# Optimization experiments

Measured on AMD Instinct MI355X. Metric: run time of the kernel, lower is better.

Reference implementation:

```python
import jax, jax.numpy as jnp
import numpy as np

B, S, D = 128, 256, 128
VOCAB, NH, K = 21, 4, 4
DI = 2 * D            # mLSTM inner dim (proj_factor=2)
QKB = 8               # qkv_proj_blocksize
NB = DI // QKB        # 32 block-diagonal qkv blocks
DHM = DI // NH        # 64 = mLSTM head dim
DHS = D // NH         # 32 = sLSTM head dim
FFU = 2 * D           # gated FFN up dim (proj_factor=2.0)


def _ln(x, w, eps=1e-5):
    mu = x.mean(-1, keepdims=True)
    var = x.var(-1, keepdims=True)
    return (x - mu) / jnp.sqrt(var + eps) * w


def _mh_ln(x, w, nh, eps=1e-5):
    # multi-head (group) layernorm: normalize each head's channels, scale by per-channel w
    b, s, d = x.shape
    xh = x.reshape(b, s, nh, d // nh)
    mu = xh.mean(-1, keepdims=True)
    var = xh.var(-1, keepdims=True)
    xn = (xh - mu) / jnp.sqrt(var + eps)
    return xn.reshape(b, s, d) * w


def _causal_conv(x, w, bias):
    # depthwise causal conv1d: x (B,S,C), w (C,K), left-pad K-1
    s = x.shape[1]
    k = w.shape[1]
    xp = jnp.pad(x, ((0, 0), (k - 1, 0), (0, 0)))
    return sum(xp[:, j:j + s, :] * w[:, j] for j in range(k)) + bias


def _blockdiag(x, w):
    # block-diagonal (headwise) linear: x (B,S,D), w (nb, out_per_block, in_per_block)
    b, s, d = x.shape
    nb = w.shape[0]
    xh = x.reshape(b, s, nb, d // nb)
    return jnp.einsum('bshd,hed->bshe', xh, w).reshape(b, s, -1)


def _mlstm_parallel(q, k, v, ip, fp, eps=1e-6):
    # parallel stabilized mLSTM; q,k,v (B,NH,S,DH); ip,fp (B,NH,S,1)
    b, nh, s, dh = q.shape
    log_f = jax.nn.log_sigmoid(fp)
    lf_cum = jnp.concatenate([jnp.zeros((b, nh, 1, 1), q.dtype),
                              jnp.cumsum(log_f, axis=2)], axis=2)      # (B,NH,S+1,1)
    m = lf_cum - jnp.swapaxes(lf_cum, -2, -1)                          # (B,NH,S+1,S+1)
    ltr = jnp.tril(jnp.ones((s, s), bool))
    log_fg = jnp.where(ltr, m[:, :, 1:, 1:], -jnp.inf)
    log_d = log_fg + jnp.swapaxes(ip, -2, -1)                          # (B,NH,S,S)
    max_d = jnp.max(log_d, axis=-1, keepdims=True)
    dmat = jnp.exp(log_d - max_d)
    qk = jnp.einsum('bhqd,bhkd->bhqk', q, k) / (dh ** 0.5)
    c = qk * dmat
    norm = jnp.maximum(jnp.abs(c.sum(-1, keepdims=True)), jnp.exp(-max_d))
    return jnp.einsum('bhqk,bhkd->bhqd', c / (norm + eps), v)


def _slstm_scan(gi, gf, gz, go, rec_w, bias):
    # sLSTM recurrence; g* (B,S,NH,DH); rec_w (NH,DH,4*DH); bias (NH,4*DH)
    b, s, nh, dh = gi.shape
    bi, bf, bz, bo = jnp.split(bias, 4, axis=-1)

    def step(carry, inp):
        h, c, n, m = carry
        ixt, fxt, zxt, oxt = inp
        rec = jnp.einsum('bhd,hde->bhe', h, rec_w)
        ri, rf, rz, ro = jnp.split(rec, 4, axis=-1)
        iraw = ixt + ri + bi
        fraw = fxt + rf + bf
        zraw = zxt + rz + bz
        oraw = oxt + ro + bo
        logfplusm = m + jax.nn.log_sigmoid(fraw)
        mnew = jnp.maximum(iraw, logfplusm)
        ig = jnp.exp(iraw - mnew)
        fg = jnp.exp(logfplusm - mnew)
        cnew = fg * c + ig * jnp.tanh(zraw)
        nnew = fg * n + ig
        hnew = jax.nn.sigmoid(oraw) * cnew / nnew
        return (hnew, cnew, nnew, mnew), hnew

    init = tuple(jnp.zeros((b, nh, dh), gi.dtype) for _ in range(4))
    xs = tuple(jnp.moveaxis(t, 1, 0) for t in (gi, gf, gz, go))
    _, ys = jax.lax.scan(step, init, xs)
    return jnp.moveaxis(ys, 0, 1)  # (B,S,NH,DH)


def _forward(x, emb, m_ln_w, m_up_w, m_conv_w, m_conv_b, m_q_w, m_k_w, m_v_w,
             m_ig_w, m_ig_b, m_fg_w, m_fg_b, m_on_w, m_skip, m_down_w,
             s_ln1_w, s_conv_w, s_conv_b, s_ig_w, s_fg_w, s_zg_w, s_og_w,
             s_rec_w, s_bias, s_gn_w, s_ln2_w, s_ff_up_w, s_ff_down_w,
             post_norm_w):
    h = emb[x]  # (B,S,D)
    # ---- block 0: mLSTM block (pre-LN residual) ----
    xn = _ln(h, m_ln_w)
    x_in, z = jnp.split(xn @ m_up_w.T, 2, axis=-1)          # each (B,S,DI)
    xca = jax.nn.silu(_causal_conv(x_in, m_conv_w, m_conv_b))
    q = _blockdiag(xca, m_q_w)
    kk = _blockdiag(xca, m_k_w)
    v = _blockdiag(x_in, m_v_w)
    ifin = jnp.concatenate([q, kk, v], axis=-1)             # (B,S,3*DI)
    ip = jnp.swapaxes(ifin @ m_ig_w.T + m_ig_b, 1, 2)[..., None]  # (B,NH,S,1)
    fp = jnp.swapaxes(ifin @ m_fg_w.T + m_fg_b, 1, 2)[..., None]
    to_heads = lambda t: jnp.swapaxes(t.reshape(B, S, NH, DHM), 1, 2)
    ht = _mlstm_parallel(to_heads(q), to_heads(kk), to_heads(v), ip, fp)
    hm = jnp.swapaxes(ht, 1, 2).reshape(B, S, DI)
    hm = _mh_ln(hm, m_on_w, NH)
    hm = (hm + m_skip * xca) * jax.nn.silu(z)
    h = h + hm @ m_down_w.T
    # ---- blocks 1,2: sLSTM blocks (pre-LN residual + gated gelu FFN) ----
    for i in range(2):
        xn = _ln(h, s_ln1_w[i])
        xc = jax.nn.silu(_causal_conv(xn, s_conv_w[i], s_conv_b[i]))
        gi = _blockdiag(xc, s_ig_w[i]).reshape(B, S, NH, DHS)
        gf = _blockdiag(xc, s_fg_w[i]).reshape(B, S, NH, DHS)
        gz = _blockdiag(xn, s_zg_w[i]).reshape(B, S, NH, DHS)
        go = _blockdiag(xn, s_og_w[i]).reshape(B, S, NH, DHS)
        y = _slstm_scan(gi, gf, gz, go, s_rec_w[i], s_bias[i])
        h = h + _mh_ln(y.reshape(B, S, D), s_gn_w[i], NH)
        xn2 = _ln(h, s_ln2_w[i])
        gate, up = jnp.split(xn2 @ s_ff_up_w[i].T, 2, axis=-1)
        h = h + (jax.nn.gelu(gate, approximate=False) * up) @ s_ff_down_w[i].T
    return _ln(h, post_norm_w)


def setup_inputs():
    key = jax.random.key(0)
    ks = iter(jax.random.split(key, 64))
    r = lambda shape, s=0.02: jax.random.normal(next(ks), shape, jnp.float32) * s
    inp = {}
    inp['x'] = jax.random.randint(next(ks), (B, S), 0, VOCAB)
    inp['emb'] = r((VOCAB, D)).at[0].set(0.0)  # padding_idx=0
    inp['m_ln_w'] = jnp.ones((D,), jnp.float32)
    inp['m_up_w'] = r((2 * DI, D))
    inp['m_conv_w'] = r((DI, K), 0.1)
    inp['m_conv_b'] = jnp.zeros((DI,), jnp.float32)
    inp['m_q_w'] = r((NB, QKB, QKB), 0.1)
    inp['m_k_w'] = r((NB, QKB, QKB), 0.1)
    inp['m_v_w'] = r((NB, QKB, QKB), 0.1)
    inp['m_ig_w'] = r((NH, 3 * DI))
    inp['m_ig_b'] = r((NH,), 0.1)
    inp['m_fg_w'] = r((NH, 3 * DI))
    inp['m_fg_b'] = jnp.linspace(3.0, 6.0, NH)  # forget-gate bias init
    inp['m_on_w'] = jnp.ones((DI,), jnp.float32)
    inp['m_skip'] = jnp.ones((DI,), jnp.float32)
    inp['m_down_w'] = r((D, DI))
    inp['s_ln1_w'] = jnp.ones((2, D), jnp.float32)
    inp['s_conv_w'] = r((2, D, K), 0.1)
    inp['s_conv_b'] = jnp.zeros((2, D), jnp.float32)
    inp['s_ig_w'] = r((2, NH, DHS, DHS), 0.05)
    inp['s_fg_w'] = r((2, NH, DHS, DHS), 0.05)
    inp['s_zg_w'] = r((2, NH, DHS, DHS), 0.05)
    inp['s_og_w'] = r((2, NH, DHS, DHS), 0.05)
    inp['s_rec_w'] = r((2, NH, DHS, 4 * DHS), 0.05)
    inp['s_bias'] = jnp.zeros((2, NH, 4 * DHS), jnp.float32).at[:, :, DHS:2 * DHS].set(jnp.linspace(3.0, 6.0, DHS))
    inp['s_gn_w'] = jnp.ones((2, D), jnp.float32)
    inp['s_ln2_w'] = jnp.ones((2, D), jnp.float32)
    inp['s_ff_up_w'] = r((2, 2 * FFU, D))
    inp['s_ff_down_w'] = r((2, D, FFU))
    inp['post_norm_w'] = jnp.ones((D,), jnp.float32)
    return inp


def reference(x, emb, m_ln_w, m_up_w, m_conv_w, m_conv_b, m_q_w, m_k_w, m_v_w,
              m_ig_w, m_ig_b, m_fg_w, m_fg_b, m_on_w, m_skip, m_down_w,
              s_ln1_w, s_conv_w, s_conv_b, s_ig_w, s_fg_w, s_zg_w, s_og_w,
              s_rec_w, s_bias, s_gn_w, s_ln2_w, s_ff_up_w, s_ff_down_w,
              post_norm_w):
    return _forward(x, emb, m_ln_w, m_up_w, m_conv_w, m_conv_b, m_q_w, m_k_w, m_v_w,
                    m_ig_w, m_ig_b, m_fg_w, m_fg_b, m_on_w, m_skip, m_down_w,
                    s_ln1_w, s_conv_w, s_conv_b, s_ig_w, s_fg_w, s_zg_w, s_og_w,
                    s_rec_w, s_bias, s_gn_w, s_ln2_w, s_ff_up_w, s_ff_down_w,
                    post_norm_w)
```

## Files before the change

### kernel.cpp

```cpp
#include <hip/hip_runtime.h>
#include <hip/hip_bf16.h>

#define BB 128
#define SS 256
#define DD 128
#define DI 256
#define NH 4
#define DHM 64
#define DHS 32
#define NROWS (BB*SS)

#define WAVE_SYNC() do { asm volatile("s_waitcnt lgkmcnt(0)" ::: "memory"); __builtin_amdgcn_wave_barrier(); } while (0)

typedef __attribute__((ext_vector_type(8))) short short8;
typedef __attribute__((ext_vector_type(4))) float f32x4;
typedef __attribute__((ext_vector_type(2))) int i32x2;

__device__ __forceinline__ float sigmoidf_(float x) { return 1.f / (1.f + __expf(-x)); }
__device__ __forceinline__ float siluf_(float x) { return x / (1.f + __expf(-x)); }
__device__ __forceinline__ float logsigf_(float x) {
    return (x >= 0.f) ? -log1pf(__expf(-x)) : x - log1pf(__expf(x));
}
__device__ __forceinline__ float geluf_(float g) {
    return 0.5f * g * (1.f + erff(g * 0.70710678118654752f));
}
__device__ __forceinline__ ushort bf16u(float x) {
    unsigned u = __float_as_uint(x);
    u += 0x7fffu + ((u >> 16) & 1u);
    return (ushort)(u >> 16);
}
__device__ __forceinline__ float ubf(ushort v) {
    return __uint_as_float((unsigned)v << 16);
}
__device__ __forceinline__ float rdlane(float v, int lane) {
    return __int_as_float(__builtin_amdgcn_readlane(__float_as_int(v), lane));
}
#define DPPADD(x, ctrl) ((x) + __int_as_float(__builtin_amdgcn_update_dpp(0, __float_as_int(x), (ctrl), 0xf, 0xf, true)))

__global__ __launch_bounds__(256) void wprep_kernel(const float* __restrict__ m_up_w,
        const float* __restrict__ m_down_w, const float* __restrict__ s_ff_up_w,
        const float* __restrict__ s_ff_down_w, const float* __restrict__ wi,
        const float* __restrict__ wf, const float* __restrict__ wz,
        const float* __restrict__ wo, const float* __restrict__ igw,
        const float* __restrict__ fgw,
        ushort* __restrict__ upb, ushort* __restrict__ downb,
        ushort* __restrict__ ffupb, ushort* __restrict__ ffdownb,
        ushort* __restrict__ sgwb, ushort* __restrict__ w16b) {
    int gid = blockIdx.x * 256 + threadIdx.x;
    if (gid < 65536) {
        upb[gid] = bf16u(m_up_w[gid]);
    } else if (gid < 98304) {
        int i = gid - 65536;
        downb[i] = bf16u(m_down_w[i]);
    } else if (gid < 229376) {
        int i = gid - 98304;
        ffupb[i] = bf16u(s_ff_up_w[i]);
    } else if (gid < 294912) {
        int i = gid - 229376;
        ffdownb[i] = bf16u(s_ff_down_w[i]);
    } else if (gid < 557056) {
        int idx = gid - 294912;
        int t = idx & 127;
        int oc = (idx >> 7) & 255;
        int pair = (idx >> 15) & 1;
        int i2 = idx >> 16;
        int h = oc >> 6, l = oc & 63, gate = (l >> 5) & 1, e = l & 31;
        const float* w = pair == 0 ? (gate == 0 ? wi : wf) : (gate == 0 ? wz : wo);
        float val = ((t >> 5) == h) ? w[i2 * 4096 + h * 1024 + e * 32 + (t & 31)] : 0.f;
        sgwb[idx] = bf16u(val);
    } else if (gid < 569344) {
        int idx = gid - 557056;
        int t = idx % 768, j = idx / 768;
        float v = 0.f;
        if (j < 4) v = igw[j * 768 + t];
        else if (j < 8) v = fgw[(j - 4) * 768 + t];
        w16b[idx] = bf16u(v);
    }
}

__global__ __launch_bounds__(256) void embed_ln_kernel(const int* __restrict__ x,
        const float* __restrict__ emb, const float* __restrict__ w,
        float* __restrict__ h, ushort* __restrict__ outb) {
    int row = blockIdx.x * 4 + (threadIdx.x >> 6);
    int lane = threadIdx.x & 63;
    int tok = x[row];
    float a = emb[tok * DD + lane], b = emb[tok * DD + 64 + lane];
    h[(size_t)row * DD + lane] = a;
    h[(size_t)row * DD + 64 + lane] = b;
    float s1 = a + b, s2 = a * a + b * b;
    #pragma unroll
    for (int o = 32; o; o >>= 1) { s1 += __shfl_xor(s1, o); s2 += __shfl_xor(s2, o); }
    float mu = s1 * (1.f / 128.f);
    float var = s2 * (1.f / 128.f) - mu * mu;
    float inv = rsqrtf(var + 1e-5f);
    ushort* brow = outb + (size_t)row * DD;
    brow[lane] = bf16u((a - mu) * inv * w[lane]);
    brow[lane + 64] = bf16u((b - mu) * inv * w[lane + 64]);
}

__global__ __launch_bounds__(256) void ln128_kernel(const float* __restrict__ x,
        const float* __restrict__ w, float* __restrict__ out, ushort* __restrict__ outb) {
    int row = blockIdx.x * 4 + (threadIdx.x >> 6);
    int lane = threadIdx.x & 63;
    const float* xr = x + (size_t)row * DD;
    float a = xr[lane], b = xr[lane + 64];
    float s1 = a + b, s2 = a * a + b * b;
    #pragma unroll
    for (int o = 32; o; o >>= 1) { s1 += __shfl_xor(s1, o); s2 += __shfl_xor(s2, o); }
    float mu = s1 * (1.f / 128.f);
    float var = s2 * (1.f / 128.f) - mu * mu;
    float inv = rsqrtf(var + 1e-5f);
    float va = (a - mu) * inv * w[lane];
    float vb = (b - mu) * inv * w[lane + 64];
    if (out) {
        float* orow = out + (size_t)row * DD;
        orow[lane] = va; orow[lane + 64] = vb;
    }
    if (outb) {
        ushort* brow = outb + (size_t)row * DD;
        brow[lane] = bf16u(va); brow[lane + 64] = bf16u(vb);
    }
}

__global__ __launch_bounds__(256) void ln_conv_s_kernel(const float* __restrict__ hsrc,
        const float* __restrict__ lnw, const float* __restrict__ cw,
        const float* __restrict__ cb, ushort* __restrict__ xnb, ushort* __restrict__ xcb) {
    __shared__ ushort lnbuf[67][128];
    int blk = blockIdx.x;
    int st = blk & 3, b = blk >> 2;
    int r0 = st * 64;
    int tid = threadIdx.x;
    int wv = tid >> 6, lane = tid & 63;
    #pragma unroll
    for (int p = 0; p < 17; ++p) {
        int rl = p * 4 + wv;
        if (rl < 67) {
            int s = r0 - 3 + rl;
            if (s >= 0) {
                const float* xr = hsrc + ((size_t)(b * 256 + s)) * 128;
                float a = xr[lane], c2 = xr[lane + 64];
                float s1 = a + c2, s2 = a * a + c2 * c2;
                #pragma unroll
                for (int o = 32; o; o >>= 1) { s1 += __shfl_xor(s1, o); s2 += __shfl_xor(s2, o); }
                float mu = s1 * (1.f / 128.f);
                float var = s2 * (1.f / 128.f) - mu * mu;
                float inv = rsqrtf(var + 1e-5f);
                lnbuf[rl][lane] = bf16u((a - mu) * inv * lnw[lane]);
                lnbuf[rl][lane + 64] = bf16u((c2 - mu) * inv * lnw[lane + 64]);
            } else {
                lnbuf[rl][lane] = 0;
                lnbuf[rl][lane + 64] = 0;
            }
        }
    }
    __syncthreads();
    int ch = tid & 127;
    int half = tid >> 7;
    float w0 = cw[ch * 4 + 0], w1 = cw[ch * 4 + 1], w2 = cw[ch * 4 + 2], w3 = cw[ch * 4 + 3];
    float bias = cb[ch];
    #pragma unroll 4
    for (int i = 0; i < 32; ++i) {
        int rr = half * 32 + i;
        int rl = 3 + rr;
        float acc = bias
            + ubf(lnbuf[rl - 3][ch]) * w0
            + ubf(lnbuf[rl - 2][ch]) * w1
            + ubf(lnbuf[rl - 1][ch]) * w2
            + ubf(lnbuf[rl][ch]) * w3;
        size_t gr = (size_t)(b * 256 + r0 + rr);
        xcb[gr * 128 + ch] = bf16u(siluf_(acc));
        xnb[gr * 128 + ch] = lnbuf[rl][ch];
    }
}

__global__ __launch_bounds__(256, 2) void gemm_bf16_kernel(const ushort* __restrict__ A, int lda,
        const ushort* __restrict__ W, float* __restrict__ C, ushort* __restrict__ Cb,
        int ldc, int K, int addC) {
    __shared__ ushort As[128 * 32];
    __shared__ ushort Bs[128 * 32];
    int m0 = blockIdx.x * 128;
    int n0 = blockIdx.y * 128;
    int tid = threadIdx.x;
    int wv = tid >> 6, l = tid & 63;
    int lr = l & 15, lg = l >> 4, g4 = lg * 4;
    int wr = wv >> 1, wc = wv & 1;
    int sr = tid >> 1;
    int sc = (tid & 1) * 2;

    f32x4 acc[4][4] = {};
    for (int k0 = 0; k0 < K; k0 += 32) {
        __syncthreads();
        #pragma unroll
        for (int u = 0; u < 2; ++u) {
            int c = sc + u;
            uint4 av = *(const uint4*)(A + (size_t)(m0 + sr) * lda + k0 + c * 8);
            *(uint4*)(As + sr * 32 + ((c ^ (sr & 3)) * 8)) = av;
            uint4 wv4 = *(const uint4*)(W + (size_t)(n0 + sr) * K + k0 + c * 8);
            *(uint4*)(Bs + sr * 32 + ((c ^ (sr & 3)) * 8)) = wv4;
        }
        __syncthreads();
        short8 af[4], bf[4];
        #pragma unroll
        for (int fm = 0; fm < 4; ++fm) {
            int row = wr * 64 + fm * 16 + lr;
            af[fm] = *(const short8*)(As + row * 32 + ((lg ^ (row & 3)) * 8));
        }
        #pragma unroll
        for (int fn = 0; fn < 4; ++fn) {
            int row = wc * 64 + fn * 16 + lr;
            bf[fn] = *(const short8*)(Bs + row * 32 + ((lg ^ (row & 3)) * 8));
        }
        #pragma unroll
        for (int fm = 0; fm < 4; ++fm)
            #pragma unroll
            for (int fn = 0; fn < 4; ++fn)
                acc[fm][fn] = __builtin_amdgcn_mfma_f32_16x16x32_bf16(af[fm], bf[fn], acc[fm][fn], 0, 0, 0);
    }
    #pragma unroll
    for (int fm = 0; fm < 4; ++fm) {
        #pragma unroll
        for (int fn = 0; fn < 4; ++fn) {
            #pragma unroll
            for (int r = 0; r < 4; ++r) {
                size_t idx = (size_t)(m0 + wr * 64 + fm * 16 + g4 + r) * ldc + n0 + wc * 64 + fn * 16 + lr;
                if (Cb) Cb[idx] = bf16u(acc[fm][fn][r]);
                else if (addC) C[idx] += acc[fm][fn][r];
                else C[idx] = acc[fm][fn][r];
            }
        }
    }
}

__global__ __launch_bounds__(256, 2) void sgate_gemm_kernel(const ushort* __restrict__ xcb,
        const ushort* __restrict__ xnb, const ushort* __restrict__ Wif,
        const ushort* __restrict__ Wzo, ushort* __restrict__ gifb, ushort* __restrict__ gzob) {
    __shared__ ushort As[128 * 32];
    __shared__ ushort Bs[128 * 32];
    int y = blockIdx.y;
    const ushort* A = (y < 2) ? xcb : xnb;
    const ushort* W = (y < 2) ? Wif : Wzo;
    ushort* Cb = (y < 2) ? gifb : gzob;
    int m0 = blockIdx.x * 128;
    int n0 = (y & 1) * 128;
    int tid = threadIdx.x;
    int wv = tid >> 6, l = tid & 63;
    int lr = l & 15, lg = l >> 4, g4 = lg * 4;
    int wr = wv >> 1, wc = wv & 1;
    int sr = tid >> 1;
    int sc = (tid & 1) * 2;

    f32x4 acc[4][4] = {};
    for (int k0 = 0; k0 < 128; k0 += 32) {
        __syncthreads();
        #pragma unroll
        for (int u = 0; u < 2; ++u) {
            int c = sc + u;
            uint4 av = *(const uint4*)(A + (size_t)(m0 + sr) * 128 + k0 + c * 8);
            *(uint4*)(As + sr * 32 + ((c ^ (sr & 3)) * 8)) = av;
            uint4 wv4 = *(const uint4*)(W + (size_t)(n0 + sr) * 128 + k0 + c * 8);
            *(uint4*)(Bs + sr * 32 + ((c ^ (sr & 3)) * 8)) = wv4;
        }
        __syncthreads();
        short8 af[4], bf[4];
        #pragma unroll
        for (int fm = 0; fm < 4; ++fm) {
            int row = wr * 64 + fm * 16 + lr;
            af[fm] = *(const short8*)(As + row * 32 + ((lg ^ (row & 3)) * 8));
        }
        #pragma unroll
        for (int fn = 0; fn < 4; ++fn) {
            int row = wc * 64 + fn * 16 + lr;
            bf[fn] = *(const short8*)(Bs + row * 32 + ((lg ^ (row & 3)) * 8));
        }
        #pragma unroll
        for (int fm = 0; fm < 4; ++fm)
            #pragma unroll
            for (int fn = 0; fn < 4; ++fn)
                acc[fm][fn] = __builtin_amdgcn_mfma_f32_16x16x32_bf16(af[fm], bf[fn], acc[fm][fn], 0, 0, 0);
    }
    #pragma unroll
    for (int fm = 0; fm < 4; ++fm)
        #pragma unroll
        for (int fn = 0; fn < 4; ++fn)
            #pragma unroll
            for (int r = 0; r < 4; ++r) {
                size_t idx = (size_t)(m0 + wr * 64 + fm * 16 + g4 + r) * 256 + n0 + wc * 64 + fn * 16 + lr;
                Cb[idx] = bf16u(acc[fm][fn][r]);
            }
}

__global__ __launch_bounds__(256, 2) void gemm_glu_kernel(const ushort* __restrict__ xzb,
        const ushort* __restrict__ W, float* __restrict__ C) {
    __shared__ ushort As[128 * 32];
    __shared__ ushort Bs[128 * 32];
    int m0 = blockIdx.x * 128;
    int tid = threadIdx.x;
    int wv = tid >> 6, l = tid & 63;
    int lr = l & 15, lg = l >> 4, g4 = lg * 4;
    int wr = wv >> 1, wc = wv & 1;
    int sr = tid >> 1;
    int sc = (tid & 1) * 2;

    f32x4 acc[4][4] = {};
    for (int k0 = 0; k0 < 256; k0 += 32) {
        __syncthreads();
        #pragma unroll
        for (int u = 0; u < 2; ++u) {
            int c = sc + u;
            short8 g8 = *(const short8*)(xzb + (size_t)(m0 + sr) * 512 + k0 + c * 8);
            short8 u8 = *(const short8*)(xzb + (size_t)(m0 + sr) * 512 + 256 + k0 + c * 8);
            short8 o8;
            #pragma unroll
            for (int t = 0; t < 8; ++t)
                o8[t] = (short)bf16u(geluf_(ubf((ushort)g8[t])) * ubf((ushort)u8[t]));
            *(short8*)(As + sr * 32 + ((c ^ (sr & 3)) * 8)) = o8;
            uint4 wv4 = *(const uint4*)(W + (size_t)sr * 256 + k0 + c * 8);
            *(uint4*)(Bs + sr * 32 + ((c ^ (sr & 3)) * 8)) = wv4;
        }
        __syncthreads();
        short8 af[4], bf[4];
        #pragma unroll
        for (int fm = 0; fm < 4; ++fm) {
            int row = wr * 64 + fm * 16 + lr;
            af[fm] = *(const short8*)(As + row * 32 + ((lg ^ (row & 3)) * 8));
        }
        #pragma unroll
        for (int fn = 0; fn < 4; ++fn) {
            int row = wc * 64 + fn * 16 + lr;
            bf[fn] = *(const short8*)(Bs + row * 32 + ((lg ^ (row & 3)) * 8));
        }
        #pragma unroll
        for (int fm = 0; fm < 4; ++fm)
            #pragma unroll
            for (int fn = 0; fn < 4; ++fn)
                acc[fm][fn] = __builtin_amdgcn_mfma_f32_16x16x32_bf16(af[fm], bf[fn], acc[fm][fn], 0, 0, 0);
    }
    #pragma unroll
    for (int fm = 0; fm < 4; ++fm)
        #pragma unroll
        for (int fn = 0; fn < 4; ++fn)
            #pragma unroll
            for (int r = 0; r < 4; ++r) {
                size_t idx = (size_t)(m0 + wr * 64 + fm * 16 + g4 + r) * 128 + wc * 64 + fn * 16 + lr;
                C[idx] += acc[fm][fn][r];
            }
}

__global__ __launch_bounds__(256) void gategemm_kernel(const ushort* __restrict__ qb,
        const ushort* __restrict__ kb, const ushort* __restrict__ vb,
        const ushort* __restrict__ W16, const float* __restrict__ igb,
        const float* __restrict__ fgb, float* __restrict__ ip, float* __restrict__ fp) {
    int tid = threadIdx.x;
    int wv = tid >> 6, l = tid & 63;
    int lr = l & 15, lg = l >> 4, g4 = lg * 4;
    int row0 = blockIdx.x * 128 + wv * 32;
    f32x4 acc[2] = {};
    #pragma unroll
    for (int k0 = 0; k0 < 768; k0 += 32) {
        short8 bfr = *(const short8*)(W16 + lr * 768 + k0 + lg * 8);
        #pragma unroll
        for (int mi = 0; mi < 2; ++mi) {
            int row = row0 + mi * 16 + lr;
            int b = row >> 8, s = row & 255;
            const ushort* src;
            size_t addr;
            if (k0 < 256) {
                src = qb;
                addr = ((size_t)(b * 4 + (k0 >> 6)) * 256 + s) * 64 + (k0 & 63) + lg * 8;
            } else if (k0 < 512) {
                int kq = k0 - 256;
                src = kb;
                addr = ((size_t)(b * 4 + (kq >> 6)) * 256 + s) * 64 + (kq & 63) + lg * 8;
            } else {
                src = vb;
                addr = (size_t)row * 256 + (k0 - 512) + lg * 8;
            }
            short8 afr = *(const short8*)(src + addr);
            acc[mi] = __builtin_amdgcn_mfma_f32_16x16x32_bf16(afr, bfr, acc[mi], 0, 0, 0);
        }
    }
    if (lr < 8) {
        float bias = (lr < 4) ? igb[lr] : fgb[lr - 4];
        float* dst = (lr < 4) ? ip : fp;
        int hh = lr & 3;
        #pragma unroll
        for (int mi = 0; mi < 2; ++mi) {
            #pragma unroll
            for (int r = 0; r < 4; ++r) {
                int row = row0 + mi * 16 + g4 + r;
                int b = row >> 8, s = row & 255;
                dst[(size_t)(b * 4 + hh) * 256 + s] = acc[mi][r] + bias;
            }
        }
    }
}

__global__ __launch_bounds__(256) void mqkv_kernel(const ushort* __restrict__ xzb,
        const float* __restrict__ cw, const float* __restrict__ cb,
        const float* __restrict__ qw, const float* __restrict__ kw,
        const float* __restrict__ vw, ushort* __restrict__ xcab,
        ushort* __restrict__ qb16, ushort* __restrict__ kb16,
        ushort* __restrict__ vb16) {
    int gid = blockIdx.x * 256 + threadIdx.x;
    int oct = gid & 31;
    int row = gid >> 5;
    int s = row & 255;
    int b = row >> 8;
    float xin[4][8];
    #pragma unroll
    for (int j = 0; j < 4; ++j) {
        int ss = s - 3 + j;
        if (ss >= 0) {
            short8 v8 = *(const short8*)(xzb + ((size_t)row + j - 3) * 512 + oct * 8);
            #pragma unroll
            for (int t = 0; t < 8; ++t) xin[j][t] = ubf((ushort)v8[t]);
        } else {
            #pragma unroll
            for (int t = 0; t < 8; ++t) xin[j][t] = 0.f;
        }
    }
    float xc8[8];
    #pragma unroll
    for (int t = 0; t < 8; ++t) {
        int ch = oct * 8 + t;
        float acc = cb[ch];
        #pragma unroll
        for (int j = 0; j < 4; ++j) acc += xin[j][t] * cw[ch * 4 + j];
        xc8[t] = siluf_(acc);
    }
    short8 qs, ks, vs, xs;
    #pragma unroll
    for (int e = 0; e < 8; ++e) {
        const float* qw8 = qw + (size_t)(oct * 8 + e) * 8;
        const float* kw8 = kw + (size_t)(oct * 8 + e) * 8;
        const float* vw8 = vw + (size_t)(oct * 8 + e) * 8;
        float aq = 0.f, ak = 0.f, av = 0.f;
        #pragma unroll
        for (int t = 0; t < 8; ++t) {
            aq += xc8[t] * qw8[t];
            ak += xc8[t] * kw8[t];
            av += xin[3][t] * vw8[t];
        }
        qs[e] = (short)bf16u(aq);
        ks[e] = (short)bf16u(ak);
        vs[e] = (short)bf16u(av);
        xs[e] = (short)bf16u(xc8[e]);
    }
    *(short8*)(xcab + (size_t)row * 256 + oct * 8) = xs;
    *(short8*)(vb16 + (size_t)row * 256 + oct * 8) = vs;
    int h2 = oct >> 3, dd = (oct & 7) * 8;
    size_t be = ((size_t)(b * 4 + h2) * 256 + s) * 64 + dd;
    *(short8*)(qb16 + be) = qs;
    *(short8*)(kb16 + be) = ks;
}

__global__ __launch_bounds__(64) void mprep_kernel(const float* __restrict__ ip,
        const float* __restrict__ fp, float* __restrict__ L,
        float* __restrict__ E, float* __restrict__ PM) {
    int bh = blockIdx.x;
    int lane = threadIdx.x;
    size_t base = (size_t)bh * SS + lane * 4;
    float lsv[4], ipv[4];
    #pragma unroll
    for (int u = 0; u < 4; ++u) {
        lsv[u] = logsigf_(fp[base + u]);
        ipv[u] = ip[base + u];
    }
    float p0 = lsv[0], p1 = p0 + lsv[1], p2 = p1 + lsv[2], p3 = p2 + lsv[3];
    float inc = p3;
    #pragma unroll
    for (int o = 1; o < 64; o <<= 1) {
        float wv = __shfl_up(inc, o);
        if (lane >= o) inc += wv;
    }
    float excl = inc - p3;
    float Lv[4] = {excl + p0, excl + p1, excl + p2, excl + p3};
    float Ev[4];
    #pragma unroll
    for (int u = 0; u < 4; ++u) Ev[u] = ipv[u] - Lv[u];
    float q0 = Ev[0], q1 = fmaxf(q0, Ev[1]), q2 = fmaxf(q1, Ev[2]), q3 = fmaxf(q2, Ev[3]);
    float incm = q3;
    #pragma unroll
    for (int o = 1; o < 64; o <<= 1) {
        float wv = __shfl_up(incm, o);
        if (lane >= o) incm = fmaxf(incm, wv);
    }
    float exm = __shfl_up(incm, 1);
    if (lane == 0) exm = -INFINITY;
    float qv[4] = {q0, q1, q2, q3};
    #pragma unroll
    for (int u = 0; u < 4; ++u) {
        L[base + u] = Lv[u];
        E[base + u] = Ev[u];
        PM[base + u] = fmaxf(exm, qv[u]);
    }
}

__global__ __launch_bounds__(256) void vtrans_kernel(const ushort* __restrict__ vb,
        ushort* __restrict__ vt) {
    int blk = blockIdx.x;
    int st = blk & 3, bh = blk >> 2;
    int b = bh >> 2, h = bh & 3;
    int tid = threadIdx.x;
    __shared__ ushort tile[64][68];
    int s0 = st * 64;
    #pragma unroll
    for (int u = 0; u < 16; ++u) {
        int idx = u * 256 + tid;
        int sl = idx >> 6, dl = idx & 63;
        tile[sl][dl] = vb[((size_t)(b * 256 + s0 + sl)) * 256 + h * 64 + dl];
    }
    __syncthreads();
    #pragma unroll
    for (int u = 0; u < 16; ++u) {
        int idx = u * 256 + tid;
        int dl = idx >> 6, sl = idx & 63;
        vt[((size_t)bh * 64 + dl) * 256 + s0 + sl] = tile[sl][dl];
    }
}

__global__ __launch_bounds__(256, 2) void mlstm_mfma_kernel(
        const ushort* __restrict__ qb, const ushort* __restrict__ kb,
        const ushort* __restrict__ vt, const float* __restrict__ Lg,
        const float* __restrict__ Eg, const float* __restrict__ PMg,
        const ushort* __restrict__ xzb, const ushort* __restrict__ xcab,
        const float* __restrict__ onw, const float* __restrict__ skip,
        ushort* __restrict__ outb) {
    int bh = blockIdx.x;
    int b = bh >> 2, h = bh & 3;
    int tid = threadIdx.x;
    int wv = tid >> 6, l = tid & 63;
    int lr = l & 15, lg = l >> 4, g4 = lg * 4;

    __shared__ ushort Kb[16384];
    __shared__ ushort Vt[16384];
    __shared__ ushort Pl[4 * 640];
    __shared__ float sE[SS], sPM[SS], sL[SS];

    const size_t gb16 = (size_t)bh * 16384;
    #pragma unroll
    for (int p2 = 0; p2 < 8; ++p2) {
        int id = p2 * 256 + tid;
        int r = id >> 3, c = id & 7;
        uint4 kval = *(const uint4*)(kb + gb16 + r * 64 + c * 8);
        *(uint4*)(Kb + r * 64 + ((c ^ (r & 7)) * 8)) = kval;
        int d = id >> 5, c2 = id & 31;
        uint4 vval = *(const uint4*)(vt + gb16 + d * 256 + c2 * 8);
        *(uint4*)(Vt + d * 256 + ((c2 ^ (d & 7)) * 8)) = vval;
    }
    sE[tid]  = Eg[(size_t)bh * SS + tid];
    sPM[tid] = PMg[(size_t)bh * SS + tid];
    sL[tid]  = Lg[(size_t)bh * SS + tid];
    __syncthreads();

    float onwv[4], skipv[4];
    #pragma unroll
    for (int dc = 0; dc < 4; ++dc) {
        int ch = h * 64 + dc * 16 + lr;
        onwv[dc] = onw[ch];
        skipv[dc] = skip[ch];
    }

    f32x4 O[4][4] = {};
    float csum[4][4] = {};
    const int pmap[4] = {wv, 7 - wv, 8 + wv, 15 - wv};
    ushort* Pw = Pl + wv * 640;

    #pragma unroll
    for (int rf = 0; rf < 4; ++rf) {
        int p = pmap[rf];
        int r0 = p * 16;
        short8 qf0 = *(const short8*)(qb + gb16 + (r0 + lr) * 64 + lg * 8);
        short8 qf1 = *(const short8*)(qb + gb16 + (r0 + lr) * 64 + 32 + lg * 8);
        float pmv[4], lv[4];
        #pragma unroll
        for (int r = 0; r < 4; ++r) { pmv[r] = sPM[r0 + g4 + r]; lv[r] = sL[r0 + g4 + r]; }
        int jtmax = r0 >> 5;
        #pragma unroll 1
        for (int jt = 0; jt <= jtmax; ++jt) {
            int jb = jt * 32;
            f32x4 s0 = {0.f, 0.f, 0.f, 0.f}, s1 = {0.f, 0.f, 0.f, 0.f};
            {
                int j = jb + lr;
                int sw = j & 7;
                short8 k00 = *(const short8*)(Kb + j * 64 + ((lg)     ^ sw) * 8);
                short8 k01 = *(const short8*)(Kb + j * 64 + ((4 + lg) ^ sw) * 8);
                int j2 = jb + 16 + lr;
                int sw2 = j2 & 7;
                short8 k10 = *(const short8*)(Kb + j2 * 64 + ((lg)     ^ sw2) * 8);
                short8 k11 = *(const short8*)(Kb + j2 * 64 + ((4 + lg) ^ sw2) * 8);
                s0 = __builtin_amdgcn_mfma_f32_16x16x32_bf16(qf0, k00, s0, 0, 0, 0);
                s0 = __builtin_amdgcn_mfma_f32_16x16x32_bf16(qf1, k01, s0, 0, 0, 0);
                s1 = __builtin_amdgcn_mfma_f32_16x16x32_bf16(qf0, k10, s1, 0, 0, 0);
                s1 = __builtin_amdgcn_mfma_f32_16x16x32_bf16(qf1, k11, s1, 0, 0, 0);
            }
            float e0 = sE[jb + lr], e1 = sE[jb + 16 + lr];
            int j0 = jb + lr, j1 = jb + 16 + lr;
            #pragma unroll
            for (int r = 0; r < 4; ++r) {
                int i = r0 + g4 + r;
                float sc0 = (j0 <= i) ? s0[r] * 0.125f * __expf(e0 - pmv[r]) : 0.f;
                float sc1 = (j1 <= i) ? s1[r] * 0.125f * __expf(e1 - pmv[r]) : 0.f;
                csum[rf][r] += sc0 + sc1;
                Pw[(g4 + r) * 40 + lr] = bf16u(sc0);
                Pw[(g4 + r) * 40 + 16 + lr] = bf16u(sc1);
            }
            WAVE_SYNC();
            short8 pf = *(const short8*)(Pw + lr * 40 + lg * 8);
            #pragma unroll
            for (int dc = 0; dc < 4; ++dc) {
                int d = dc * 16 + lr;
                int chunk = (jt * 4 + lg) ^ (d & 7);
                short8 vf = *(const short8*)(Vt + d * 256 + chunk * 8);
                O[rf][dc] = __builtin_amdgcn_mfma_f32_16x16x32_bf16(pf, vf, O[rf][dc], 0, 0, 0);
            }
        }
        #pragma unroll
        for (int r = 0; r < 4; ++r) {
            float cs = csum[rf][r];
            cs += __shfl_xor(cs, 1); cs += __shfl_xor(cs, 2);
            cs += __shfl_xor(cs, 4); cs += __shfl_xor(cs, 8);
            float nrm = fmaxf(fabsf(cs), __expf(-(lv[r] + pmv[r]))) + 1e-6f;
            float rinv = 1.f / nrm;
            float v0 = O[rf][0][r] * rinv, v1 = O[rf][1][r] * rinv;
            float v2 = O[rf][2][r] * rinv, v3 = O[rf][3][r] * rinv;
            float s1m = v0 + v1 + v2 + v3;
            float s2m = v0 * v0 + v1 * v1 + v2 * v2 + v3 * v3;
            s1m += __shfl_xor(s1m, 1); s2m += __shfl_xor(s2m, 1);
            s1m += __shfl_xor(s1m, 2); s2m += __shfl_xor(s2m, 2);
            s1m += __shfl_xor(s1m, 4); s2m += __shfl_xor(s2m, 4);
            s1m += __shfl_xor(s1m, 8); s2m += __shfl_xor(s2m, 8);
            float mu = s1m * (1.f / 64.f);
            float var = s2m * (1.f / 64.f) - mu * mu;
            float inv = rsqrtf(var + 1e-5f);
            int grow = b * 256 + r0 + g4 + r;
            float vv[4] = {v0, v1, v2, v3};
            #pragma unroll
            for (int dc = 0; dc < 4; ++dc) {
                int ch = h * 64 + dc * 16 + lr;
                float z = ubf(xzb[(size_t)grow * 512 + 256 + ch]);
                float xnv = (vv[dc] - mu) * inv * onwv[dc];
                float val = (xnv + skipv[dc] * ubf(xcab[(size_t)grow * 256 + ch])) * siluf_(z);
                outb[(size_t)grow * 256 + ch] = bf16u(val);
            }
        }
    }
}

__global__ __launch_bounds__(64, 1) void slstm_scan_kernel(const ushort* __restrict__ gifb,
        const ushort* __restrict__ gzob, const float* __restrict__ rec_w,
        const float* __restrict__ bias, const float* __restrict__ gnw,
        float* __restrict__ hbuf) {
    int bh = blockIdx.x;
    int b = bh >> 2, h = bh & 3;
    int l = threadIdx.x;
    int c = l & 31;
    bool lo = (l < 32);
    unsigned wpk[32];
    const float* wp = rec_w + (size_t)h * 4096 + l;
    #pragma unroll
    for (int d = 0; d < 32; ++d) {
        float w0v = wp[d * 128];
        float w1v = wp[d * 128 + 64];
        wpk[d] = ((unsigned)bf16u(w1v) << 16) | (unsigned)bf16u(w0v);
    }
    float b0 = bias[h * 128 + l];
    float b1 = bias[h * 128 + 64 + l];
    float gw = gnw[h * 32 + c];
    float cst = 0.f, nst = 0.f, hreg = 0.f;
    size_t gb = (size_t)b * SS * 256 + h * 64 + l;
    size_t hb = (size_t)b * SS * 128 + h * 32 + c;
    float pg0[4], pg1[4], ph[4];
    #pragma unroll
    for (int u = 0; u < 4; ++u) {
        pg0[u] = ubf(gifb[gb + (size_t)u * 256]);
        pg1[u] = ubf(gzob[gb + (size_t)u * 256]);
        ph[u]  = hbuf[hb + (size_t)u * 128];
    }
    float pend_hv = 0.f, pend_hcur = 0.f;
    int pend_off = 0;
    for (int s = 0; s < SS; s += 4) {
        #pragma unroll
        for (int u = 0; u < 4; ++u) {
            float a00 = 0.f, a01 = 0.f, a02 = 0.f, a03 = 0.f;
            float a10 = 0.f, a11 = 0.f, a12 = 0.f, a13 = 0.f;
            #pragma unroll
            for (int d = 0; d < 32; d += 4) {
                float h0 = rdlane(hreg, d);
                float h1 = rdlane(hreg, d + 1);
                float h2 = rdlane(hreg, d + 2);
                float h3 = rdlane(hreg, d + 3);
                unsigned p0 = wpk[d], p1 = wpk[d + 1], p2 = wpk[d + 2], p3 = wpk[d + 3];
                a00 += __uint_as_float(p0 << 16) * h0;
                a10 += __uint_as_float(p0) * h0;
                a01 += __uint_as_float(p1 << 16) * h1;
                a11 += __uint_as_float(p1) * h1;
                a02 += __uint_as_float(p2 << 16) * h2;
                a12 += __uint_as_float(p2) * h2;
                a03 += __uint_as_float(p3 << 16) * h3;
                a13 += __uint_as_float(p3) * h3;
            }
            float raw0 = pg0[u] + ((a00 + a01) + (a02 + a03)) + b0;
            float raw1 = pg1[u] + ((a10 + a11) + (a12 + a13)) + b1;
            float hcur = ph[u];
            {
                float s1 = pend_hv, s2 = pend_hv * pend_hv;
                s1 = DPPADD(s1, 0x111); s2 = DPPADD(s2, 0x111);
                s1 = DPPADD(s1, 0x112); s2 = DPPADD(s2, 0x112);
                s1 = DPPADD(s1, 0x114); s2 = DPPADD(s2, 0x114);
                s1 = DPPADD(s1, 0x118); s2 = DPPADD(s2, 0x118);
                s1 = DPPADD(s1, 0x142); s2 = DPPADD(s2, 0x142);
                s1 = DPPADD(s1, 0x143); s2 = DPPADD(s2, 0x143);
                float mu = rdlane(s1, 63) * (1.f / 64.f);
                float var = rdlane(s2, 63) * (1.f / 64.f) - mu * mu;
                float outv = (pend_hv - mu) * rsqrtf(var + 1e-5f) * gw;
                if (lo) hbuf[hb + (size_t)pend_off * 128] = pend_hcur + outv;
            }
            int s4 = s + 4 + u;
            if (s4 < SS) {
                pg0[u] = ubf(gifb[gb + (size_t)s4 * 256]);
                pg1[u] = ubf(gzob[gb + (size_t)s4 * 256]);
                ph[u]  = hbuf[hb + (size_t)s4 * 128];
            }
            i32x2 r0p = __builtin_amdgcn_permlane32_swap(__float_as_int(raw0), __float_as_int(raw0), false, false);
            i32x2 r1p = __builtin_amdgcn_permlane32_swap(__float_as_int(raw1), __float_as_int(raw1), false, false);
            float q0 = __int_as_float(lo ? r0p.y : r0p.x);
            float q1 = __int_as_float(lo ? r1p.y : r1p.x);
            float iraw = lo ? raw0 : q0;
            float zraw = lo ? raw1 : q1;
            float fraw = lo ? q0 : raw0;
            float oraw = lo ? q1 : raw1;
            float fg = __builtin_amdgcn_rcpf(1.f + __expf(-fraw));
            float ig = __expf(iraw);
            float e2z = __expf(2.f * zraw);
            float tz = 1.f - 2.f * __builtin_amdgcn_rcpf(e2z + 1.f);
            cst = fg * cst + ig * tz;
            nst = fg * nst + ig;
            float sg = __builtin_amdgcn_rcpf(1.f + __expf(-oraw));
            float hv = sg * cst * __builtin_amdgcn_rcpf(nst);
            hreg = hv;
            pend_hv = hv;
            pend_hcur = hcur;
            pend_off = s + u;
        }
    }
    {
        float s1 = pend_hv, s2 = pend_hv * pend_hv;
        s1 = DPPADD(s1, 0x111); s2 = DPPADD(s2, 0x111);
        s1 = DPPADD(s1, 0x112); s2 = DPPADD(s2, 0x112);
        s1 = DPPADD(s1, 0x114); s2 = DPPADD(s2, 0x114);
        s1 = DPPADD(s1, 0x118); s2 = DPPADD(s2, 0x118);
        s1 = DPPADD(s1, 0x142); s2 = DPPADD(s2, 0x142);
        s1 = DPPADD(s1, 0x143); s2 = DPPADD(s2, 0x143);
        float mu = rdlane(s1, 63) * (1.f / 64.f);
        float var = rdlane(s2, 63) * (1.f / 64.f) - mu * mu;
        float outv = (pend_hv - mu) * rsqrtf(var + 1e-5f) * gw;
        if (lo) hbuf[hb + (size_t)pend_off * 128] = pend_hcur + outv;
    }
}

extern "C" void kernel_launch(void* const* d_in, const int* in_sizes, int n_in,
                              void* d_out, int out_size, void* d_ws, size_t ws_size,
                              hipStream_t stream) {
    const int*   x        = (const int*)d_in[0];
    const float* emb      = (const float*)d_in[1];
    const float* m_ln_w   = (const float*)d_in[2];
    const float* m_up_w   = (const float*)d_in[3];
    const float* m_conv_w = (const float*)d_in[4];
    const float* m_conv_b = (const float*)d_in[5];
    const float* m_q_w    = (const float*)d_in[6];
    const float* m_k_w    = (const float*)d_in[7];
    const float* m_v_w    = (const float*)d_in[8];
    const float* m_ig_w   = (const float*)d_in[9];
    const float* m_ig_b   = (const float*)d_in[10];
    const float* m_fg_w   = (const float*)d_in[11];
    const float* m_fg_b   = (const float*)d_in[12];
    const float* m_on_w   = (const float*)d_in[13];
    const float* m_skip   = (const float*)d_in[14];
    const float* m_down_w = (const float*)d_in[15];
    const float* s_ln1_w  = (const float*)d_in[16];
    const float* s_conv_w = (const float*)d_in[17];
    const float* s_conv_b = (const float*)d_in[18];
    const float* s_ig_w   = (const float*)d_in[19];
    const float* s_fg_w   = (const float*)d_in[20];
    const float* s_zg_w   = (const float*)d_in[21];
    const float* s_og_w   = (const float*)d_in[22];
    const float* s_rec_w  = (const float*)d_in[23];
    const float* s_bias   = (const float*)d_in[24];
    const float* s_gn_w   = (const float*)d_in[25];
    const float* s_ln2_w  = (const float*)d_in[26];
    const float* s_ff_up_w   = (const float*)d_in[27];
    const float* s_ff_down_w = (const float*)d_in[28];
    const float* post_norm_w = (const float*)d_in[29];
    float* out = (float*)d_out;

    float* ws = (float*)d_ws;
    const size_t NR = NROWS;
    float* h   = ws;
    float* regA = h   + NR * 128;
    float* regB = regA + NR * 128;
    float* gip = regB + NR * 128;
    float* gfp = gip + 512 * 256;
    float* gL  = gfp + 512 * 256;
    float* gE  = gL  + 512 * 256;
    float* gPM = gE  + 512 * 256;
    float* extra = gPM + 512 * 256;
    ushort* xnb   = (ushort*)extra;
    ushort* xzb   = xnb + NR * 128;
    ushort* xcab  = xzb + NR * 512;
    ushort* qb16  = xcab + NR * 256;
    ushort* vb16  = qb16 + NR * 256;
    ushort* upb   = vb16 + NR * 256;
    ushort* downb = upb + 512 * 128;
    ushort* ffupb = downb + 128 * 256;
    ushort* ffdownb = ffupb + 2 * 512 * 128;
    ushort* sgwb  = ffdownb + 2 * 128 * 256;
    ushort* w16b  = sgwb + 2 * 2 * 256 * 128;
    ushort* kb16   = (ushort*)out;
    ushort* vtb    = (ushort*)regA;
    ushort* gifb   = (ushort*)regA;
    ushort* mpostb = (ushort*)regB;
    ushort* gzob   = (ushort*)regB;
    ushort* xcb    = qb16;

    wprep_kernel<<<(569344 + 255) / 256, 256, 0, stream>>>(m_up_w, m_down_w, s_ff_up_w,
            s_ff_down_w, s_ig_w, s_fg_w, s_zg_w, s_og_w, m_ig_w, m_fg_w,
            upb, downb, ffupb, ffdownb, sgwb, w16b);

    embed_ln_kernel<<<NR / 4, 256, 0, stream>>>(x, emb, m_ln_w, h, xnb);
    gemm_bf16_kernel<<<dim3(NR / 128, 4), 256, 0, stream>>>(xnb, 128, upb, nullptr, xzb, 512, 128, 0);
    mqkv_kernel<<<(NR * 32) / 256, 256, 0, stream>>>(xzb, m_conv_w, m_conv_b,
            m_q_w, m_k_w, m_v_w, xcab, qb16, kb16, vb16);
    gategemm_kernel<<<NR / 128, 256, 0, stream>>>(qb16, kb16, vb16, w16b, m_ig_b, m_fg_b, gip, gfp);
    mprep_kernel<<<BB * NH, 64, 0, stream>>>(gip, gfp, gL, gE, gPM);
    vtrans_kernel<<<BB * NH * 4, 256, 0, stream>>>(vb16, vtb);
    mlstm_mfma_kernel<<<BB * NH, 256, 0, stream>>>(qb16, kb16, vtb, gL, gE, gPM,
            xzb, xcab, m_on_w, m_skip, mpostb);
    gemm_bf16_kernel<<<dim3(NR / 128, 1), 256, 0, stream>>>(mpostb, 256, downb, h, nullptr, 128, 256, 1);

    for (int i2 = 0; i2 < 2; ++i2) {
        ln_conv_s_kernel<<<BB * 4, 256, 0, stream>>>(h, s_ln1_w + i2 * 128,
                s_conv_w + i2 * 128 * 4, s_conv_b + i2 * 128, xnb, xcb);
        sgate_gemm_kernel<<<dim3(NR / 128, 4), 256, 0, stream>>>(xcb, xnb,
                sgwb + (size_t)(i2 * 2 + 0) * 256 * 128, sgwb + (size_t)(i2 * 2 + 1) * 256 * 128,
                gifb, gzob);
        slstm_scan_kernel<<<BB * NH, 64, 0, stream>>>(gifb, gzob,
                s_rec_w + i2 * 4 * 32 * 128, s_bias + i2 * 4 * 128, s_gn_w + i2 * 128, h);
        ln128_kernel<<<NR / 4, 256, 0, stream>>>(h, s_ln2_w + i2 * 128, nullptr, xnb);
        gemm_bf16_kernel<<<dim3(NR / 128, 4), 256, 0, stream>>>(xnb, 128, ffupb + (size_t)i2 * 512 * 128, nullptr, xzb, 512, 128, 0);
        gemm_glu_kernel<<<NR / 128, 256, 0, stream>>>(xzb, ffdownb + (size_t)i2 * 128 * 256, h);
    }
    ln128_kernel<<<NR / 4, 256, 0, stream>>>(h, post_norm_w, out, nullptr);
}
```

Measured before the change: 683.0 us.

## Batch 16 sequences per wave in sLSTM scan using MFMA recurrent matmul

The sLSTM scan kernel now handles 16 batch rows per wave for one head, and computes the recurrent h·R product with bf16 16x16x32 MFMA instructions instead of per-lane readlane FMAs. The hidden state moves through a small LDS tile, and the gate weight layout is interleaved (i/f, z/o pairs) so each lane reads both gates with a single 32-bit load. The grid drops from 512 single-wave blocks to 32, cutting the total serial FMA work but leaving far fewer waves to hide latency on a GPU with many CUs. The recurrent state is also rounded to bf16 before the MFMA, which costs precision.

```diff
diff --git a/kernel.cpp b/kernel.cpp
--- a/kernel.cpp
+++ b/kernel.cpp
@@ -32,10 +32,6 @@
 __device__ __forceinline__ float ubf(ushort v) {
     return __uint_as_float((unsigned)v << 16);
 }
-__device__ __forceinline__ float rdlane(float v, int lane) {
-    return __int_as_float(__builtin_amdgcn_readlane(__float_as_int(v), lane));
-}
-#define DPPADD(x, ctrl) ((x) + __int_as_float(__builtin_amdgcn_update_dpp(0, __float_as_int(x), (ctrl), 0xf, 0xf, true)))
 
 __global__ __launch_bounds__(256) void wprep_kernel(const float* __restrict__ m_up_w,
         const float* __restrict__ m_down_w, const float* __restrict__ s_ff_up_w,
@@ -64,7 +60,7 @@
         int oc = (idx >> 7) & 255;
         int pair = (idx >> 15) & 1;
         int i2 = idx >> 16;
-        int h = oc >> 6, l = oc & 63, gate = (l >> 5) & 1, e = l & 31;
+        int h = oc >> 6, l = oc & 63, gate = l & 1, e = l >> 1;
         const float* w = pair == 0 ? (gate == 0 ? wi : wf) : (gate == 0 ? wz : wo);
         float val = ((t >> 5) == h) ? w[i2 * 4096 + h * 1024 + e * 32 + (t & 31)] : 0.f;
         sgwb[idx] = bf16u(val);
@@ -651,111 +647,134 @@
         const ushort* __restrict__ gzob, const float* __restrict__ rec_w,
         const float* __restrict__ bias, const float* __restrict__ gnw,
         float* __restrict__ hbuf) {
-    int bh = blockIdx.x;
-    int b = bh >> 2, h = bh & 3;
+    int blk = blockIdx.x;
+    int h = blk >> 3;
+    int b0 = (blk & 7) * 16;
     int l = threadIdx.x;
-    int c = l & 31;
-    bool lo = (l < 32);
-    unsigned wpk[32];
-    const float* wp = rec_w + (size_t)h * 4096 + l;
-    #pragma unroll
-    for (int d = 0; d < 32; ++d) {
-        float w0v = wp[d * 128];
-        float w1v = wp[d * 128 + 64];
-        wpk[d] = ((unsigned)bf16u(w1v) << 16) | (unsigned)bf16u(w0v);
-    }
-    float b0 = bias[h * 128 + l];
-    float b1 = bias[h * 128 + 64 + l];
-    float gw = gnw[h * 32 + c];
-    float cst = 0.f, nst = 0.f, hreg = 0.f;
-    size_t gb = (size_t)b * SS * 256 + h * 64 + l;
-    size_t hb = (size_t)b * SS * 128 + h * 32 + c;
-    float pg0[4], pg1[4], ph[4];
-    #pragma unroll
-    for (int u = 0; u < 4; ++u) {
-        pg0[u] = ubf(gifb[gb + (size_t)u * 256]);
-        pg1[u] = ubf(gzob[gb + (size_t)u * 256]);
-        ph[u]  = hbuf[hb + (size_t)u * 128];
-    }
-    float pend_hv = 0.f, pend_hcur = 0.f;
-    int pend_off = 0;
-    for (int s = 0; s < SS; s += 4) {
-        #pragma unroll
-        for (int u = 0; u < 4; ++u) {
-            float a00 = 0.f, a01 = 0.f, a02 = 0.f, a03 = 0.f;
-            float a10 = 0.f, a11 = 0.f, a12 = 0.f, a13 = 0.f;
-            #pragma unroll
-            for (int d = 0; d < 32; d += 4) {
-                float h0 = rdlane(hreg, d);
-                float h1 = rdlane(hreg, d + 1);
-                float h2 = rdlane(hreg, d + 2);
-                float h3 = rdlane(hreg, d + 3);
-                unsigned p0 = wpk[d], p1 = wpk[d + 1], p2 = wpk[d + 2], p3 = wpk[d + 3];
-                a00 += __uint_as_float(p0 << 16) * h0;
-                a10 += __uint_as_float(p0) * h0;
-                a01 += __uint_as_float(p1 << 16) * h1;
-                a11 += __uint_as_float(p1) * h1;
-                a02 += __uint_as_float(p2 << 16) * h2;
-                a12 += __uint_as_float(p2) * h2;
-                a03 += __uint_as_float(p3 << 16) * h3;
-                a13 += __uint_as_float(p3) * h3;
-            }
-            float raw0 = pg0[u] + ((a00 + a01) + (a02 + a03)) + b0;
-            float raw1 = pg1[u] + ((a10 + a11) + (a12 + a13)) + b1;
-            float hcur = ph[u];
+    int c = l & 15, g = l >> 4;
+    __shared__ ushort hlds[16][36];
+
+    short8 wf[8];
+    #pragma unroll
+    for (int t = 0; t < 8; ++t)
+        #pragma unroll
+        for (int j = 0; j < 8; ++j)
+            wf[t][j] = (short)bf16u(rec_w[(size_t)h * 4096 + (size_t)(8 * g + j) * 128 + 16 * t + c]);
+
+    int ch0 = c, ch1 = c + 16;
+    float bi0 = bias[h * 128 + ch0],      bi1 = bias[h * 128 + ch1];
+    float bf0 = bias[h * 128 + 32 + ch0], bf1 = bias[h * 128 + 32 + ch1];
+    float bz0 = bias[h * 128 + 64 + ch0], bz1 = bias[h * 128 + 64 + ch1];
+    float bo0 = bias[h * 128 + 96 + ch0], bo1 = bias[h * 128 + 96 + ch1];
+    float gw0 = gnw[h * 32 + ch0],        gw1 = gnw[h * 32 + ch1];
+
+    size_t gbase[4], hbase[4];
+    #pragma unroll
+    for (int r = 0; r < 4; ++r) {
+        int b = b0 + 4 * g + r;
+        gbase[r] = (size_t)b * 256 * 256 + h * 64;
+        hbase[r] = (size_t)b * 256 * 128 + h * 32;
+    }
+
+    for (int i = l; i < 288; i += 64) ((uint*)hlds)[i] = 0;
+    WAVE_SYNC();
+
+    float cs0[4] = {}, cs1[4] = {}, ns0[4] = {}, ns1[4] = {};
+
+    uint pif0[4], pif1[4], pzo0[4], pzo1[4];
+    #pragma unroll
+    for (int r = 0; r < 4; ++r) {
+        pif0[r] = *(const uint*)(gifb + gbase[r] + 2 * ch0);
+        pif1[r] = *(const uint*)(gifb + gbase[r] + 2 * ch1);
+        pzo0[r] = *(const uint*)(gzob + gbase[r] + 2 * ch0);
+        pzo1[r] = *(const uint*)(gzob + gbase[r] + 2 * ch1);
+    }
+
+    for (int s = 0; s < SS; ++s) {
+        union { short8 s8; uint2 u2[2]; } af;
+        af.u2[0] = *(const uint2*)&hlds[c][8 * g];
+        af.u2[1] = *(const uint2*)&hlds[c][8 * g + 4];
+        f32x4 zero = {0.f, 0.f, 0.f, 0.f};
+        f32x4 m0 = __builtin_amdgcn_mfma_f32_16x16x32_bf16(af.s8, wf[0], zero, 0, 0, 0);
+        f32x4 m1 = __builtin_amdgcn_mfma_f32_16x16x32_bf16(af.s8, wf[1], zero, 0, 0, 0);
+        f32x4 m2 = __builtin_amdgcn_mfma_f32_16x16x32_bf16(af.s8, wf[2], zero, 0, 0, 0);
+        f32x4 m3 = __builtin_amdgcn_mfma_f32_16x16x32_bf16(af.s8, wf[3], zero, 0, 0, 0);
+        f32x4 m4 = __builtin_amdgcn_mfma_f32_16x16x32_bf16(af.s8, wf[4], zero, 0, 0, 0);
+        f32x4 m5 = __builtin_amdgcn_mfma_f32_16x16x32_bf16(af.s8, wf[5], zero, 0, 0, 0);
+        f32x4 m6 = __builtin_amdgcn_mfma_f32_16x16x32_bf16(af.s8, wf[6], zero, 0, 0, 0);
+        f32x4 m7 = __builtin_amdgcn_mfma_f32_16x16x32_bf16(af.s8, wf[7], zero, 0, 0, 0);
+        float hc0[4], hc1[4];
+        #pragma unroll
+        for (int r = 0; r < 4; ++r) {
+            hc0[r] = hbuf[hbase[r] + (size_t)s * 128 + ch0];
+            hc1[r] = hbuf[hbase[r] + (size_t)s * 128 + ch1];
+        }
+        uint nif0[4], nif1[4], nzo0[4], nzo1[4];
+        if (s < SS - 1) {
+            size_t so = (size_t)(s + 1) * 256;
+            #pragma unroll
+            for (int r = 0; r < 4; ++r) {
+                nif0[r] = *(const uint*)(gifb + gbase[r] + so + 2 * ch0);
+                nif1[r] = *(const uint*)(gifb + gbase[r] + so + 2 * ch1);
+                nzo0[r] = *(const uint*)(gzob + gbase[r] + so + 2 * ch0);
+                nzo1[r] = *(const uint*)(gzob + gbase[r] + so + 2 * ch1);
+            }
+        }
+        float hv0[4], hv1[4];
+        #pragma unroll
+        for (int r = 0; r < 4; ++r) {
             {
-                float s1 = pend_hv, s2 = pend_hv * pend_hv;
-                s1 = DPPADD(s1, 0x111); s2 = DPPADD(s2, 0x111);
-                s1 = DPPADD(s1, 0x112); s2 = DPPADD(s2, 0x112);
-                s1 = DPPADD(s1, 0x114); s2 = DPPADD(s2, 0x114);
-                s1 = DPPADD(s1, 0x118); s2 = DPPADD(s2, 0x118);
-                s1 = DPPADD(s1, 0x142); s2 = DPPADD(s2, 0x142);
-                s1 = DPPADD(s1, 0x143); s2 = DPPADD(s2, 0x143);
-                float mu = rdlane(s1, 63) * (1.f / 64.f);
-                float var = rdlane(s2, 63) * (1.f / 64.f) - mu * mu;
-                float outv = (pend_hv - mu) * rsqrtf(var + 1e-5f) * gw;
-                if (lo) hbuf[hb + (size_t)pend_off * 128] = pend_hcur + outv;
-            }
-            int s4 = s + 4 + u;
-            if (s4 < SS) {
-                pg0[u] = ubf(gifb[gb + (size_t)s4 * 256]);
-                pg1[u] = ubf(gzob[gb + (size_t)s4 * 256]);
-                ph[u]  = hbuf[hb + (size_t)s4 * 128];
-            }
-            i32x2 r0p = __builtin_amdgcn_permlane32_swap(__float_as_int(raw0), __float_as_int(raw0), false, false);
-            i32x2 r1p = __builtin_amdgcn_permlane32_swap(__float_as_int(raw1), __float_as_int(raw1), false, false);
-            float q0 = __int_as_float(lo ? r0p.y : r0p.x);
-            float q1 = __int_as_float(lo ? r1p.y : r1p.x);
-            float iraw = lo ? raw0 : q0;
-            float zraw = lo ? raw1 : q1;
-            float fraw = lo ? q0 : raw0;
-            float oraw = lo ? q1 : raw1;
-            float fg = __builtin_amdgcn_rcpf(1.f + __expf(-fraw));
-            float ig = __expf(iraw);
-            float e2z = __expf(2.f * zraw);
-            float tz = 1.f - 2.f * __builtin_amdgcn_rcpf(e2z + 1.f);
-            cst = fg * cst + ig * tz;
-            nst = fg * nst + ig;
-            float sg = __builtin_amdgcn_rcpf(1.f + __expf(-oraw));
-            float hv = sg * cst * __builtin_amdgcn_rcpf(nst);
-            hreg = hv;
-            pend_hv = hv;
-            pend_hcur = hcur;
-            pend_off = s + u;
-        }
-    }
-    {
-        float s1 = pend_hv, s2 = pend_hv * pend_hv;
-        s1 = DPPADD(s1, 0x111); s2 = DPPADD(s2, 0x111);
-        s1 = DPPADD(s1, 0x112); s2 = DPPADD(s2, 0x112);
-        s1 = DPPADD(s1, 0x114); s2 = DPPADD(s2, 0x114);
-        s1 = DPPADD(s1, 0x118); s2 = DPPADD(s2, 0x118);
-        s1 = DPPADD(s1, 0x142); s2 = DPPADD(s2, 0x142);
-        s1 = DPPADD(s1, 0x143); s2 = DPPADD(s2, 0x143);
-        float mu = rdlane(s1, 63) * (1.f / 64.f);
-        float var = rdlane(s2, 63) * (1.f / 64.f) - mu * mu;
-        float outv = (pend_hv - mu) * rsqrtf(var + 1e-5f) * gw;
-        if (lo) hbuf[hb + (size_t)pend_off * 128] = pend_hcur + outv;
+                float iraw = m0[r] + ubf((ushort)(pif0[r] & 0xffffu)) + bi0;
+                float fraw = m2[r] + ubf((ushort)(pif0[r] >> 16)) + bf0;
+                float zraw = m4[r] + ubf((ushort)(pzo0[r] & 0xffffu)) + bz0;
+                float oraw = m6[r] + ubf((ushort)(pzo0[r] >> 16)) + bo0;
+                float fg = __builtin_amdgcn_rcpf(1.f + __expf(-fraw));
+                float ig = __expf(iraw);
+                float tz = 1.f - 2.f * __builtin_amdgcn_rcpf(__expf(2.f * zraw) + 1.f);
+                cs0[r] = fg * cs0[r] + ig * tz;
+                ns0[r] = fg * ns0[r] + ig;
+                float sg = __builtin_amdgcn_rcpf(1.f + __expf(-oraw));
+                hv0[r] = sg * cs0[r] * __builtin_amdgcn_rcpf(ns0[r]);
+            }
+            {
+                float iraw = m1[r] + ubf((ushort)(pif1[r] & 0xffffu)) + bi1;
+                float fraw = m3[r] + ubf((ushort)(pif1[r] >> 16)) + bf1;
+                float zraw = m5[r] + ubf((ushort)(pzo1[r] & 0xffffu)) + bz1;
+                float oraw = m7[r] + ubf((ushort)(pzo1[r] >> 16)) + bo1;
+                float fg = __builtin_amdgcn_rcpf(1.f + __expf(-fraw));
+                float ig = __expf(iraw);
+                float tz = 1.f - 2.f * __builtin_amdgcn_rcpf(__expf(2.f * zraw) + 1.f);
+                cs1[r] = fg * cs1[r] + ig * tz;
+                ns1[r] = fg * ns1[r] + ig;
+                float sg = __builtin_amdgcn_rcpf(1.f + __expf(-oraw));
+                hv1[r] = sg * cs1[r] * __builtin_amdgcn_rcpf(ns1[r]);
+            }
+        }
+        #pragma unroll
+        for (int r = 0; r < 4; ++r) {
+            hlds[4 * g + r][ch0] = bf16u(hv0[r]);
+            hlds[4 * g + r][ch1] = bf16u(hv1[r]);
+        }
+        #pragma unroll
+        for (int r = 0; r < 4; ++r) {
+            float s1 = hv0[r] + hv1[r];
+            float s2 = hv0[r] * hv0[r] + hv1[r] * hv1[r];
+            s1 += __shfl_xor(s1, 1); s2 += __shfl_xor(s2, 1);
+            s1 += __shfl_xor(s1, 2); s2 += __shfl_xor(s2, 2);
+            s1 += __shfl_xor(s1, 4); s2 += __shfl_xor(s2, 4);
+            s1 += __shfl_xor(s1, 8); s2 += __shfl_xor(s2, 8);
+            float mu = s1 * (1.f / 32.f);
+            float var = s2 * (1.f / 32.f) - mu * mu;
+            float inv = rsqrtf(var + 1e-5f);
+            hbuf[hbase[r] + (size_t)s * 128 + ch0] = hc0[r] + (hv0[r] - mu) * inv * gw0;
+            hbuf[hbase[r] + (size_t)s * 128 + ch1] = hc1[r] + (hv1[r] - mu) * inv * gw1;
+        }
+        #pragma unroll
+        for (int r = 0; r < 4; ++r) {
+            pif0[r] = nif0[r]; pif1[r] = nif1[r];
+            pzo0[r] = nzo0[r]; pzo1[r] = nzo1[r];
+        }
+        WAVE_SYNC();
     }
 }
 
@@ -844,7 +863,7 @@
         sgate_gemm_kernel<<<dim3(NR / 128, 4), 256, 0, stream>>>(xcb, xnb,
                 sgwb + (size_t)(i2 * 2 + 0) * 256 * 128, sgwb + (size_t)(i2 * 2 + 1) * 256 * 128,
                 gifb, gzob);
-        slstm_scan_kernel<<<BB * NH, 64, 0, stream>>>(gifb, gzob,
+        slstm_scan_kernel<<<32, 64, 0, stream>>>(gifb, gzob,
                 s_rec_w + i2 * 4 * 32 * 128, s_bias + i2 * 4 * 128, s_gn_w + i2 * 128, h);
         ln128_kernel<<<NR / 4, 256, 0, stream>>>(h, s_ln2_w + i2 * 128, nullptr, xnb);
         gemm_bf16_kernel<<<dim3(NR / 128, 4), 256, 0, stream>>>(xnb, 128, ffupb + (size_t)i2 * 512 * 128, nullptr, xzb, 512, 128, 0);
```

Measured after the change: 1.127 ms. 1.65x slower.
